# Optimization experiments

Hardware: AMD Instinct MI355X
Metric: run time of the kernel (lower is better)

## Reference

```python
import jax, jax.numpy as jnp
import numpy as np

N_NODES = 100000


def gcn_conv(x, edge_index, W, b):
    # GCNConv with add_self_loops=True, normalize=True (symmetric norm):
    # out = D^{-1/2} (A + I) D^{-1/2} (x @ W) + b
    n = x.shape[0]
    h = x @ W  # transform first (PyG applies lin before propagate)
    src, dst = edge_index[0], edge_index[1]
    ones = jnp.ones(src.shape[0], dtype=h.dtype)
    # degree with self-loops: in-degree + 1
    deg = jax.ops.segment_sum(ones, dst, num_segments=n) + 1.0
    dinv = jax.lax.rsqrt(deg)  # deg >= 1, always finite
    # per-edge normalized messages, scatter-add to dst
    msg = h[src] * (dinv[src] * dinv[dst])[:, None]
    agg = jax.ops.segment_sum(msg, dst, num_segments=n)
    # self-loop contribution: norm = dinv[i]^2
    agg = agg + h * (dinv * dinv)[:, None]
    return agg + b


def setup_inputs() -> dict:
    key = jax.random.key(0)
    ks = jax.random.split(key, 8)
    x = jax.random.normal(ks[0], (N_NODES, 256), dtype=jnp.float32)
    edge_index = jax.random.randint(ks[1], (2, 3200000), 0, N_NODES, dtype=jnp.int32)
    W1 = jax.random.normal(ks[2], (256, 32), dtype=jnp.float32) * (1.0 / np.sqrt(256))
    b1 = jnp.zeros((32,), dtype=jnp.float32)
    Wm = jax.random.normal(ks[3], (32, 16), dtype=jnp.float32) * (1.0 / np.sqrt(32))
    bm = jnp.zeros((16,), dtype=jnp.float32)
    Wv = jax.random.normal(ks[4], (32, 16), dtype=jnp.float32) * (1.0 / np.sqrt(32))
    bv = jnp.zeros((16,), dtype=jnp.float32)
    return {"x": x, "edge_index": edge_index, "W1": W1, "b1": b1,
            "Wm": Wm, "bm": bm, "Wv": Wv, "bv": bv}


def reference(x, edge_index, W1, b1, Wm, bm, Wv, bv):
    h = jax.nn.relu(gcn_conv(x, edge_index, W1, b1))
    mu = gcn_conv(h, edge_index, Wm, bm)
    sigma = gcn_conv(h, edge_index, Wv, bv)
    return (mu, sigma)
```

## Files before the change

### kernel.cpp

```cpp
#include <hip/hip_runtime.h>
#include <hip/hip_fp16.h>

#define NNODES 100000
#define NEDGES 3200000
#define F_IN   256
#define F_HID  32
#define F_OUT  16

#define NB   196
#define NPB  512
#define CAP  20480
#define NCHUNK 256
#define CHUNK  12500

#define GRID1 ((NNODES + 63) / 64)
#define XT_RS 130

typedef _Float16 half_t;
typedef half_t half8 __attribute__((ext_vector_type(8)));
typedef float f32x4 __attribute__((ext_vector_type(4)));
typedef const __attribute__((address_space(1))) unsigned int* gas_u32;
typedef __attribute__((address_space(3))) unsigned int* las_u32;


__global__ void k_init(int* __restrict__ bcur) {
    if (threadIdx.x < NB) bcur[threadIdx.x] = threadIdx.x * CAP;
}

__global__ __launch_bounds__(1024) void k_phaseA(
        const int* __restrict__ src, const int* __restrict__ dst,
        int* __restrict__ bcur, unsigned int* __restrict__ rec) {
    __shared__ int lh[NB];
    __shared__ int lcur[NB];
    int t = threadIdx.x;
    int e0 = blockIdx.x * CHUNK;
    if (t < NB) lh[t] = 0;
    __syncthreads();
    for (int i = t; i < CHUNK; i += 1024)
        atomicAdd(&lh[dst[e0 + i] >> 9], 1);
    __syncthreads();
    if (t < NB) lcur[t] = lh[t] ? atomicAdd(&bcur[t], lh[t]) : 0;
    __syncthreads();
    for (int i = t; i < CHUNK; i += 1024) {
        int s = src[e0 + i], d = dst[e0 + i];
        int b = d >> 9;
        int pos = atomicAdd(&lcur[b], 1);
        rec[pos] = ((unsigned)s << 9) | (unsigned)(d & 511);
    }
}

__global__ __launch_bounds__(1024) void k_phaseB(
        const unsigned int* __restrict__ rec, const int* __restrict__ bcur,
        int* __restrict__ rowptr, int* __restrict__ cnt,
        float* __restrict__ dinv, int* __restrict__ csr) {
    __shared__ int lh[NPB];
    __shared__ int lsc[NPB];
    __shared__ int wsum[16];
    int t = threadIdx.x, b = blockIdx.x;
    int lo = b * CAP, hi = bcur[b];
    if (t < NPB) lh[t] = 0;
    __syncthreads();
    for (int i = lo + t; i < hi; i += 1024)
        atomicAdd(&lh[rec[i] & 511], 1);
    __syncthreads();
    int lane = t & 63, w = t >> 6;
    int my = (t < NPB) ? lh[t] : 0;
    int v = my;
    #pragma unroll
    for (int d = 1; d < 64; d <<= 1) {
        int tmp = __shfl_up(v, d, 64);
        if (lane >= d) v += tmp;
    }
    if (lane == 63) wsum[w] = v;
    __syncthreads();
    if (w == 0) {
        int s = (lane < 16) ? wsum[lane] : 0;
        #pragma unroll
        for (int d = 1; d < 16; d <<= 1) {
            int tmp = __shfl_up(s, d, 64);
            if (lane >= d) s += tmp;
        }
        if (lane < 16) wsum[lane] = s;
    }
    __syncthreads();
    int ex = v + (w > 0 ? wsum[w - 1] : 0) - my;
    int node = b * NPB + t;
    if (t < NPB) {
        lsc[t] = ex;
        if (node < NNODES) {
            rowptr[node] = lo + ex;
            cnt[node] = my;
            dinv[node] = rsqrtf((float)my + 1.0f);
        }
    }
    __syncthreads();
    for (int i = lo + t; i < hi; i += 1024) {
        unsigned r = rec[i];
        int dl = r & 511;
        int p = atomicAdd(&lsc[dl], 1);
        csr[lo + p] = (int)(r >> 9);
    }
}


__global__ __launch_bounds__(256) void k_gemm1(
        const float* __restrict__ x, const float* __restrict__ W1,
        const float* __restrict__ dinv, __half2* __restrict__ g1) {
    __shared__ half_t Wt[32 * 264];
    __shared__ float xt[4][16 * XT_RS];
    int t = threadIdx.x;
    int wave = t >> 6, lane = t & 63;
    int m = lane & 15, q = lane >> 4;
    int row0 = blockIdx.x * 64 + wave * 16;

    for (int i = t; i < F_IN * F_HID; i += 256) {
        int k = i >> 5, f = i & 31;
        Wt[f * 264 + k] = (half_t)W1[i];
    }
    __syncthreads();

    half8 B[2][8];
    #pragma unroll
    for (int ft = 0; ft < 2; ++ft)
        #pragma unroll
        for (int kc = 0; kc < 8; ++kc)
            B[ft][kc] = *(const half8*)&Wt[(ft * 16 + m) * 264 + kc * 32 + q * 8];

    float* xw = xt[wave];
    f32x4 acc0 = {0.f, 0.f, 0.f, 0.f};
    f32x4 acc1 = {0.f, 0.f, 0.f, 0.f};
    #pragma unroll
    for (int kh = 0; kh < 2; ++kh) {
        #pragma unroll
        for (int r = 0; r < 16; ++r) {
            int grow = row0 + r; if (grow >= NNODES) grow = NNODES - 1;
            const float* gp = &x[(size_t)grow * F_IN + kh * 128 + lane];
            __builtin_amdgcn_global_load_lds((gas_u32)gp,
                (las_u32)&xw[r * XT_RS], 4, 0, 0);
            __builtin_amdgcn_global_load_lds((gas_u32)(gp + 64),
                (las_u32)&xw[r * XT_RS + 64], 4, 0, 0);
        }
        asm volatile("s_waitcnt vmcnt(0)" ::: "memory");
        #pragma unroll
        for (int kc = 0; kc < 4; ++kc) {
            const float* sp = &xw[m * XT_RS + kc * 32 + q * 8];
            float2 x0 = *(const float2*)sp;
            float2 x1 = *(const float2*)(sp + 2);
            float2 x2 = *(const float2*)(sp + 4);
            float2 x3 = *(const float2*)(sp + 6);
            half8 A;
            A[0] = (half_t)x0.x; A[1] = (half_t)x0.y;
            A[2] = (half_t)x1.x; A[3] = (half_t)x1.y;
            A[4] = (half_t)x2.x; A[5] = (half_t)x2.y;
            A[6] = (half_t)x3.x; A[7] = (half_t)x3.y;
            acc0 = __builtin_amdgcn_mfma_f32_16x16x32_f16(A, B[0][kh * 4 + kc], acc0, 0, 0, 0);
            acc1 = __builtin_amdgcn_mfma_f32_16x16x32_f16(A, B[1][kh * 4 + kc], acc1, 0, 0, 0);
        }
        if (kh == 0) asm volatile("s_waitcnt lgkmcnt(0)" ::: "memory");
    }

    __syncthreads();
    float* sb = xw;
    #pragma unroll
    for (int r = 0; r < 4; ++r) {
        int rl = q * 4 + r;
        int grow = row0 + rl; if (grow >= NNODES) grow = NNODES - 1;
        float dv = dinv[grow];
        sb[rl * 33 + m]      = acc0[r] * dv;
        sb[rl * 33 + 16 + m] = acc1[r] * dv;
    }
    __syncthreads();
    int rl = (t >> 2) & 15;
    int w2 = t >> 6;
    int c0 = (t & 3) * 8;
    int grow = blockIdx.x * 64 + w2 * 16 + rl;
    if (grow < NNODES) {
        const float* sp = &xt[w2][rl * 33 + c0];
        __half2 h0 = __floats2half2_rn(sp[0], sp[1]);
        __half2 h1 = __floats2half2_rn(sp[2], sp[3]);
        __half2 h2 = __floats2half2_rn(sp[4], sp[5]);
        __half2 h3 = __floats2half2_rn(sp[6], sp[7]);
        __half2* gp = &g1[(size_t)grow * 16 + (c0 >> 1)];
        gp[0] = h0; gp[1] = h1; gp[2] = h2; gp[3] = h3;
    }
}


__global__ __launch_bounds__(256) void k_gather_l1(
        const int* __restrict__ rowptr, const int* __restrict__ cnt,
        const int* __restrict__ csr,
        const float* __restrict__ dinv, const __half2* __restrict__ g,
        const float* __restrict__ b1, const float* __restrict__ Wm,
        const float* __restrict__ Wv, __half2* __restrict__ g2) {
    __shared__ float Wcat[F_HID * 32];
    __shared__ float hrow[16][F_HID + 2];
    int tx = threadIdx.x;
    for (int idx = tx; idx < F_HID * 32; idx += 256) {
        int k = idx >> 5, j = idx & 31;
        Wcat[idx] = (j < F_OUT) ? Wm[k * F_OUT + j] : Wv[k * F_OUT + (j - F_OUT)];
    }
    int f2 = tx & 15;
    int lr = tx >> 4;
    int node = blockIdx.x * 16 + lr;
    int start = rowptr[node], end = start + cnt[node];
    float2 acc = __half22float2(g[(size_t)node * 16 + f2]);
    int j = start;
    for (; j + 4 <= end; j += 4) {
        int s0 = csr[j], s1 = csr[j + 1], s2 = csr[j + 2], s3 = csr[j + 3];
        float2 a0 = __half22float2(g[(size_t)s0 * 16 + f2]);
        float2 a1 = __half22float2(g[(size_t)s1 * 16 + f2]);
        float2 a2 = __half22float2(g[(size_t)s2 * 16 + f2]);
        float2 a3 = __half22float2(g[(size_t)s3 * 16 + f2]);
        acc.x += (a0.x + a1.x) + (a2.x + a3.x);
        acc.y += (a0.y + a1.y) + (a2.y + a3.y);
    }
    for (; j < end; ++j) {
        float2 a = __half22float2(g[(size_t)csr[j] * 16 + f2]);
        acc.x += a.x; acc.y += a.y;
    }
    float dv = dinv[node];
    float h0 = dv * acc.x + b1[2 * f2];
    float h1 = dv * acc.y + b1[2 * f2 + 1];
    hrow[lr][2 * f2]     = h0 > 0.f ? h0 : 0.f;
    hrow[lr][2 * f2 + 1] = h1 > 0.f ? h1 : 0.f;
    __syncthreads();
    float o0 = 0.f, o1 = 0.f;
    #pragma unroll
    for (int k = 0; k < F_HID; ++k) {
        float hv = hrow[lr][k];
        o0 = fmaf(hv, Wcat[k * 32 + 2 * f2], o0);
        o1 = fmaf(hv, Wcat[k * 32 + 2 * f2 + 1], o1);
    }
    g2[(size_t)node * 16 + f2] = __floats2half2_rn(o0 * dv, o1 * dv);
}


__global__ __launch_bounds__(256) void k_gather_out(
        const int* __restrict__ rowptr, const int* __restrict__ cnt,
        const int* __restrict__ csr,
        const float* __restrict__ dinv, const __half2* __restrict__ g,
        const float* __restrict__ bm, const float* __restrict__ bv,
        float* __restrict__ out) {
    int tx = threadIdx.x;
    int f2 = tx & 15;
    int node = blockIdx.x * 16 + (tx >> 4);
    int start = rowptr[node], end = start + cnt[node];
    float2 acc = __half22float2(g[(size_t)node * 16 + f2]);
    int j = start;
    for (; j + 4 <= end; j += 4) {
        int s0 = csr[j], s1 = csr[j + 1], s2 = csr[j + 2], s3 = csr[j + 3];
        float2 a0 = __half22float2(g[(size_t)s0 * 16 + f2]);
        float2 a1 = __half22float2(g[(size_t)s1 * 16 + f2]);
        float2 a2 = __half22float2(g[(size_t)s2 * 16 + f2]);
        float2 a3 = __half22float2(g[(size_t)s3 * 16 + f2]);
        acc.x += (a0.x + a1.x) + (a2.x + a3.x);
        acc.y += (a0.y + a1.y) + (a2.y + a3.y);
    }
    for (; j < end; ++j) {
        float2 a = __half22float2(g[(size_t)csr[j] * 16 + f2]);
        acc.x += a.x; acc.y += a.y;
    }
    float dv = dinv[node];
    int f = 2 * f2;
    if (f < F_OUT) {
        float2 o = { dv * acc.x + bm[f], dv * acc.y + bm[f + 1] };
        *(float2*)&out[(size_t)node * F_OUT + f] = o;
    } else {
        float2 o = { dv * acc.x + bv[f - F_OUT], dv * acc.y + bv[f - F_OUT + 1] };
        *(float2*)&out[(size_t)NNODES * F_OUT + (size_t)node * F_OUT + (f - F_OUT)] = o;
    }
}


extern "C" void kernel_launch(void* const* d_in, const int* in_sizes, int n_in,
                              void* d_out, int out_size, void* d_ws, size_t ws_size,
                              hipStream_t stream) {
    const float* x   = (const float*)d_in[0];
    const int*   ei  = (const int*)  d_in[1];
    const float* W1  = (const float*)d_in[2];
    const float* b1  = (const float*)d_in[3];
    const float* Wm  = (const float*)d_in[4];
    const float* bm  = (const float*)d_in[5];
    const float* Wv  = (const float*)d_in[6];
    const float* bv  = (const float*)d_in[7];
    float* out = (float*)d_out;

    const int* src = ei;
    const int* dst = ei + NEDGES;

    char* ws = (char*)d_ws;
    float*        dinv   = (float*)ws;        ws += 100352 * 4;
    int*          bcur   = (int*)ws;          ws += 256 * 4;
    int*          rowptr = (int*)ws;          ws += 100352 * 4;
    int*          cnt    = (int*)ws;          ws += 100352 * 4;
    int*          csr    = (int*)ws;          ws += (size_t)NB * CAP * 4;
    unsigned int* rec    = (unsigned int*)ws; ws += (size_t)NB * CAP * 4;
    __half2*      g2     = (__half2*)ws;

    __half2* g1 = (__half2*)rec;

    k_init  <<<1, 256, 0, stream>>>(bcur);
    k_phaseA<<<NCHUNK, 1024, 0, stream>>>(src, dst, bcur, rec);
    k_phaseB<<<NB, 1024, 0, stream>>>(rec, bcur, rowptr, cnt, dinv, csr);

    k_gemm1<<<GRID1, 256, 0, stream>>>(x, W1, dinv, g1);

    k_gather_l1<<<NNODES / 16, 256, 0, stream>>>(rowptr, cnt, csr, dinv, g1, b1, Wm, Wv, g2);

    k_gather_out<<<NNODES / 16, 256, 0, stream>>>(rowptr, cnt, csr, dinv, g2, bm, bv, out);
}
```

Baseline: 344.3 us.

## Cache edge records in registers across passes and split x-tile waits

The two CSR-building kernels now load their dst and record values into registers once and reuse them for both the histogram pass and the scatter pass, so global memory is read once instead of twice. In gemm1, the x-tile loads are reordered so the first 64 columns of every row are issued before the second 64. A partial vmcnt wait then lets the MFMAs on the first half start while the second half is still in flight. The fixed register arrays (RPT_A=13, RPT_B=20) raise register pressure and rely on bucket sizes never exceeding 20480 records.

```diff
diff --git a/kernel.cpp b/kernel.cpp
--- a/kernel.cpp
+++ b/kernel.cpp
@@ -12,6 +12,8 @@
 #define CAP  20480
 #define NCHUNK 256
 #define CHUNK  12500
+#define RPT_B  20
+#define RPT_A  13
 
 #define GRID1 ((NNODES + 63) / 64)
 #define XT_RS 130
@@ -35,17 +37,30 @@
     int t = threadIdx.x;
     int e0 = blockIdx.x * CHUNK;
     if (t < NB) lh[t] = 0;
-    __syncthreads();
-    for (int i = t; i < CHUNK; i += 1024)
-        atomicAdd(&lh[dst[e0 + i] >> 9], 1);
+
+    int dcache[RPT_A];
+    #pragma unroll
+    for (int k = 0; k < RPT_A; ++k) {
+        int i = t + k * 1024;
+        dcache[k] = (i < CHUNK) ? dst[e0 + i] : -1;
+    }
+    __syncthreads();
+    #pragma unroll
+    for (int k = 0; k < RPT_A; ++k)
+        if (dcache[k] >= 0) atomicAdd(&lh[dcache[k] >> 9], 1);
     __syncthreads();
     if (t < NB) lcur[t] = lh[t] ? atomicAdd(&bcur[t], lh[t]) : 0;
     __syncthreads();
-    for (int i = t; i < CHUNK; i += 1024) {
-        int s = src[e0 + i], d = dst[e0 + i];
-        int b = d >> 9;
-        int pos = atomicAdd(&lcur[b], 1);
-        rec[pos] = ((unsigned)s << 9) | (unsigned)(d & 511);
+    #pragma unroll
+    for (int k = 0; k < RPT_A; ++k) {
+        int i = t + k * 1024;
+        if (dcache[k] >= 0) {
+            int s = src[e0 + i];
+            int d = dcache[k];
+            int b = d >> 9;
+            int pos = atomicAdd(&lcur[b], 1);
+            rec[pos] = ((unsigned)s << 9) | (unsigned)(d & 511);
+        }
     }
 }
 
@@ -57,12 +72,22 @@
     __shared__ int lsc[NPB];
     __shared__ int wsum[16];
     int t = threadIdx.x, b = blockIdx.x;
-    int lo = b * CAP, hi = bcur[b];
+    int lo = b * CAP;
+    int nrec = bcur[b] - lo;
     if (t < NPB) lh[t] = 0;
-    __syncthreads();
-    for (int i = lo + t; i < hi; i += 1024)
-        atomicAdd(&lh[rec[i] & 511], 1);
-    __syncthreads();
+
+    unsigned rcache[RPT_B];
+    #pragma unroll
+    for (int k = 0; k < RPT_B; ++k) {
+        int i = t + k * 1024;
+        rcache[k] = (i < nrec) ? rec[lo + i] : 0xFFFFFFFFu;
+    }
+    __syncthreads();
+    #pragma unroll
+    for (int k = 0; k < RPT_B; ++k)
+        if (rcache[k] != 0xFFFFFFFFu) atomicAdd(&lh[rcache[k] & 511], 1);
+    __syncthreads();
+
     int lane = t & 63, w = t >> 6;
     int my = (t < NPB) ? lh[t] : 0;
     int v = my;
@@ -94,12 +119,13 @@
         }
     }
     __syncthreads();
-    for (int i = lo + t; i < hi; i += 1024) {
-        unsigned r = rec[i];
-        int dl = r & 511;
-        int p = atomicAdd(&lsc[dl], 1);
-        csr[lo + p] = (int)(r >> 9);
-    }
+    #pragma unroll
+    for (int k = 0; k < RPT_B; ++k)
+        if (rcache[k] != 0xFFFFFFFFu) {
+            int dl = rcache[k] & 511;
+            int p = atomicAdd(&lsc[dl], 1);
+            csr[lo + p] = (int)(rcache[k] >> 9);
+        }
 }
 
 
@@ -137,12 +163,18 @@
             const float* gp = &x[(size_t)grow * F_IN + kh * 128 + lane];
             __builtin_amdgcn_global_load_lds((gas_u32)gp,
                 (las_u32)&xw[r * XT_RS], 4, 0, 0);
+        }
+        #pragma unroll
+        for (int r = 0; r < 16; ++r) {
+            int grow = row0 + r; if (grow >= NNODES) grow = NNODES - 1;
+            const float* gp = &x[(size_t)grow * F_IN + kh * 128 + lane];
             __builtin_amdgcn_global_load_lds((gas_u32)(gp + 64),
                 (las_u32)&xw[r * XT_RS + 64], 4, 0, 0);
         }
-        asm volatile("s_waitcnt vmcnt(0)" ::: "memory");
         #pragma unroll
         for (int kc = 0; kc < 4; ++kc) {
+            if (kc == 0) asm volatile("s_waitcnt vmcnt(16)" ::: "memory");
+            if (kc == 2) asm volatile("s_waitcnt vmcnt(0)" ::: "memory");
             const float* sp = &xw[m * XT_RS + kc * 32 + q * 8];
             float2 x0 = *(const float2*)sp;
             float2 x1 = *(const float2*)(sp + 2);
```

New measurement: 337.5 us. 1.02x faster.
